# Kernel tuning notes

Measured on AMD Instinct MI355X. Metric: run time of the kernel, lower is better.

Reference implementation:

```python
import jax, jax.numpy as jnp
import numpy as np

HID, AA, ESM = 128, 21, 320
D1 = HID + AA + ESM          # 469
N_GRAPHS = 64
BN_EPS = 1e-5


def _lin_params(key, din, dout):
    k1, k2 = jax.random.split(key)
    s = 1.0 / np.sqrt(din)
    W = jax.random.uniform(k1, (din, dout), jnp.float32, -s, s)
    b = jax.random.uniform(k2, (dout,), jnp.float32, -s, s)
    return W, b


def setup_inputs() -> dict:
    key = jax.random.key(0)
    ks = jax.random.split(key, 16)
    N, E = 30000, 480000
    inp = {
        'prot_x': jax.random.normal(ks[0], (N, 6485), jnp.float32),
        'prot_edge_index': jax.random.randint(ks[1], (2, E), 0, N, jnp.int64),
        'prot_batch': jnp.sort(jax.random.randint(ks[2], (N,), 0, N_GRAPHS, jnp.int64)),
    }
    inp['fl1_W'], inp['fl1_b'] = _lin_params(ks[3], 6165 - 21, HID)
    inp['fl2_W'], inp['fl2_b'] = _lin_params(ks[4], AA, AA)
    inp['fl3_W'], inp['fl3_b'] = _lin_params(ks[5], ESM, ESM)
    inp['pdb1_W'], inp['pdb1_b'] = _lin_params(ks[6], D1, D1)
    inp['pdb2_W'], inp['pdb2_b'] = _lin_params(ks[7], D1, 2 * D1)
    inp['af1_W'], inp['af1_b'] = _lin_params(ks[8], D1, D1)
    inp['af2_W'], inp['af2_b'] = _lin_params(ks[9], D1, 2 * D1)
    inp['pdb3_W'], inp['pdb3_b'] = _lin_params(ks[10], 4 * D1, 4 * D1)
    inp['fc1_W'], inp['fc1_b'] = _lin_params(ks[11], 4 * D1, 1024)
    inp['bn_g'] = jnp.ones((1024,), jnp.float32)
    inp['bn_b'] = jnp.zeros((1024,), jnp.float32)
    inp['fc2_W'], inp['fc2_b'] = _lin_params(ks[12], 1024, 486)
    return inp


def _gcn_graph(edge_index, n):
    # add self-loops, symmetric normalization D^-1/2 (A+I) D^-1/2
    loops = jnp.arange(n, dtype=edge_index.dtype)
    src = jnp.concatenate([edge_index[0], loops])
    dst = jnp.concatenate([edge_index[1], loops])
    deg = jax.ops.segment_sum(jnp.ones_like(dst, jnp.float32), dst, n)
    dinv = jax.lax.rsqrt(jnp.maximum(deg, 1.0))  # deg >= 1 via self-loop
    norm = dinv[src] * dinv[dst]
    return src, dst, norm


def _gcn_conv(x, W, b, src, dst, norm, n):
    h = x @ W                                   # [N, Dout]
    msg = h[src] * norm[:, None]                # gather + scale
    return jax.ops.segment_sum(msg, dst, n) + b  # scatter-add


def reference(prot_x, prot_edge_index, prot_batch,
              fl1_W, fl1_b, fl2_W, fl2_b, fl3_W, fl3_b,
              pdb1_W, pdb1_b, pdb2_W, pdb2_b,
              af1_W, af1_b, af2_W, af2_b,
              pdb3_W, pdb3_b, fc1_W, fc1_b, bn_g, bn_b, fc2_W, fc2_b):
    n = prot_x.shape[0]
    relu = jax.nn.relu
    f1 = relu(prot_x[:, 21:6165] @ fl1_W + fl1_b)   # [N,128]
    f2 = relu(prot_x[:, :21] @ fl2_W + fl2_b)       # [N,21]
    f3 = relu(prot_x[:, 6165:] @ fl3_W + fl3_b)     # [N,320]
    feat = jnp.concatenate([f2, f1, f3], axis=1)    # [N,469]

    src, dst, norm = _gcn_graph(prot_edge_index, n)
    x = relu(_gcn_conv(feat, pdb1_W, pdb1_b, src, dst, norm, n))
    x = relu(_gcn_conv(x, pdb2_W, pdb2_b, src, dst, norm, n))
    y = relu(_gcn_conv(feat, af1_W, af1_b, src, dst, norm, n))
    y = relu(_gcn_conv(y, af2_W, af2_b, src, dst, norm, n))
    z = jnp.concatenate([x, y], axis=1)             # [N, 4*469]
    z = relu(_gcn_conv(z, pdb3_W, pdb3_b, src, dst, norm, n))

    # gap: global mean pool per graph
    cnt = jax.ops.segment_sum(jnp.ones((n,), jnp.float32), prot_batch, N_GRAPHS)
    z = jax.ops.segment_sum(z, prot_batch, N_GRAPHS) / jnp.maximum(cnt, 1.0)[:, None]

    z = z @ fc1_W + fc1_b                            # [G,1024]
    mu = jnp.mean(z, axis=0)
    var = jnp.mean((z - mu) ** 2, axis=0)            # biased, torch BN training math
    z = (z - mu) * jax.lax.rsqrt(var + BN_EPS) * bn_g + bn_b
    z = relu(z)                                      # dropout = identity (eval)
    z = z @ fc2_W + fc2_b
    return jax.nn.sigmoid(z)
```

## Files before the change

kernel.cpp:

```cpp
#include <hip/hip_runtime.h>
#include <hip/hip_bf16.h>
#include <stdint.h>

#define NG 64

typedef __attribute__((ext_vector_type(8))) short bf16x8;
typedef __attribute__((ext_vector_type(4))) float f32x4;

#define AS1 __attribute__((address_space(1)))
#define AS3 __attribute__((address_space(3)))

static __device__ __forceinline__ unsigned short f2b(float f) {
    unsigned u = __float_as_uint(f);
    return (unsigned short)((u + 0x7fffu + ((u >> 16) & 1u)) >> 16);
}
static __device__ __forceinline__ float b2f(unsigned short h) {
    return __uint_as_float(((unsigned)h) << 16);
}
static __device__ __forceinline__ void gl16(const void* g, void* l) {
    __builtin_amdgcn_global_load_lds(
        (const AS1 void*)(uintptr_t)g,
        (AS3 void*)(unsigned)(uintptr_t)l, 16, 0, 0);
}

__global__ void initdeg_k(float* deg, int* cnt, int n) {
    int i = blockIdx.x * blockDim.x + threadIdx.x;
    if (i < n) { deg[i] = 1.0f; cnt[i] = 0; }
}
__global__ void count_k(const int* __restrict__ dst, float* deg, int* cnt, int E) {
    int e = blockIdx.x * blockDim.x + threadIdx.x;
    if (e < E) { int d = dst[e]; atomicAdd(&deg[d], 1.0f); atomicAdd(&cnt[d], 1); }
}
__global__ void dinv_k(const float* __restrict__ deg, float* dinv, int n) {
    int i = blockIdx.x * blockDim.x + threadIdx.x;
    if (i < n) dinv[i] = rsqrtf(fmaxf(deg[i], 1.0f));
}
__global__ void exscan_k(const int* __restrict__ cnt, int* rowptr, int n) {
    __shared__ int tmp[1024];
    __shared__ int carry;
    int tid = threadIdx.x;
    if (tid == 0) { carry = 0; rowptr[0] = 0; }
    __syncthreads();
    for (int base = 0; base < n; base += 1024) {
        int i = base + tid;
        int v = (i < n) ? cnt[i] : 0;
        tmp[tid] = v;
        __syncthreads();
        for (int off = 1; off < 1024; off <<= 1) {
            int t = (tid >= off) ? tmp[tid - off] : 0;
            __syncthreads();
            tmp[tid] += t;
            __syncthreads();
        }
        int inc = tmp[tid] + carry;
        if (i < n) rowptr[i + 1] = inc;
        __syncthreads();
        if (tid == 1023) carry = inc;
        __syncthreads();
    }
}
__global__ void fillinit_k(const int* __restrict__ rowptr, int* fill, int n) {
    int i = blockIdx.x * blockDim.x + threadIdx.x;
    if (i < n) fill[i] = rowptr[i];
}
__global__ void fill_k(const int* __restrict__ src, const int* __restrict__ dst,
                       int* fill, int* csr, int E) {
    int e = blockIdx.x * blockDim.x + threadIdx.x;
    if (e < E) {
        int d = dst[e];
        int pos = atomicAdd(&fill[d], 1);
        csr[pos] = src[e];
    }
}

__global__ void cvt_k(const float* __restrict__ x, int ldx, int c0,
                      unsigned short* __restrict__ out, int K) {
    int kc = blockIdx.x * blockDim.x + threadIdx.x;
    int row = blockIdx.y;
    if (kc * 8 >= K) return;
    const float* src = x + (size_t)row * ldx + c0 + kc * 8;
    unsigned short t[8];
#pragma unroll
    for (int i = 0; i < 8; ++i) t[i] = f2b(src[i]);
    *(bf16x8*)(out + (size_t)row * K + kc * 8) = *(const bf16x8*)t;
}

__global__ void wtconv_k(const float* __restrict__ W, int K, int Nout,
                         unsigned short* __restrict__ Wt, int Kpad) {
    __shared__ float t[32][33];
    int k0 = blockIdx.x * 32, n0 = blockIdx.y * 32;
    int cx = threadIdx.x & 31, ry = threadIdx.x >> 5;
#pragma unroll
    for (int p = 0; p < 4; ++p) {
        int k = k0 + ry + p * 8, nn = n0 + cx;
        t[ry + p * 8][cx] = (k < K && nn < Nout) ? W[(size_t)k * Nout + nn] : 0.0f;
    }
    __syncthreads();
#pragma unroll
    for (int p = 0; p < 4; ++p) {
        int nn = n0 + ry + p * 8, k = k0 + cx;
        Wt[(size_t)nn * Kpad + k] = f2b(t[cx][ry + p * 8]);
    }
}

__global__ void fl2_k(const float* __restrict__ x, int ldx,
                      const float* __restrict__ W, const float* __restrict__ b,
                      unsigned short* __restrict__ out, int ldo, int n) {
    __shared__ float Ws[441];
    __shared__ float Bs[21];
    int tid = threadIdx.x;
    for (int i = tid; i < 441; i += 256) Ws[i] = W[i];
    if (tid < 21) Bs[tid] = b[tid];
    __syncthreads();
    int row = blockIdx.x * 256 + tid;
    if (row >= n) return;
    float xv[21];
#pragma unroll
    for (int j = 0; j < 21; ++j) xv[j] = x[(size_t)row * ldx + j];
    for (int c = 0; c < 21; ++c) {
        float a = Bs[c];
#pragma unroll
        for (int j = 0; j < 21; ++j) a = fmaf(xv[j], Ws[j * 21 + c], a);
        out[(size_t)row * ldo + c] = f2b(fmaxf(a, 0.0f));
    }
}

__global__ __launch_bounds__(256) void mgemm_k(
    const unsigned short* __restrict__ A, int lda,
    const unsigned short* __restrict__ Bt, int ldb,
    const float* __restrict__ bias,
    unsigned short* __restrict__ C, int ldc, int coff,
    int K, int Nout, int Nzero) {
    __shared__ unsigned short As[128 * 32];
    __shared__ unsigned short Bs[128 * 32];
    const int tid = threadIdx.x;
    const int w = tid >> 6, lane = tid & 63;
    const int m0 = blockIdx.y * 128, n0 = blockIdx.x * 128;
    const int wr = w >> 1, wc = w & 1;

    f32x4 acc[4][4];
#pragma unroll
    for (int i = 0; i < 4; ++i)
#pragma unroll
        for (int j = 0; j < 4; ++j) acc[i][j] = (f32x4){0.f, 0.f, 0.f, 0.f};

    const int ko = (lane >> 4) * 8;
    const int rA = wr * 64 + (lane & 15);
    const int rB = wc * 64 + (lane & 15);

    for (int k0 = 0; k0 < K; k0 += 32) {
#pragma unroll
        for (int j = 0; j < 2; ++j) {
            int c = w * 2 + j;
            int idx = c * 64 + lane;
            int row = idx >> 2, cc = idx & 3;
            gl16(A + (size_t)(m0 + row) * lda + k0 + cc * 8, &As[c * 512]);
            gl16(Bt + (size_t)(n0 + row) * ldb + k0 + cc * 8, &Bs[c * 512]);
        }
        __syncthreads();
        bf16x8 a[4], b[4];
#pragma unroll
        for (int i = 0; i < 4; ++i) {
            a[i] = *(const bf16x8*)&As[(rA + i * 16) * 32 + ko];
            b[i] = *(const bf16x8*)&Bs[(rB + i * 16) * 32 + ko];
        }
#pragma unroll
        for (int i = 0; i < 4; ++i)
#pragma unroll
            for (int j = 0; j < 4; ++j)
                acc[i][j] = __builtin_amdgcn_mfma_f32_16x16x32_bf16(a[i], b[j], acc[i][j], 0, 0, 0);
        __syncthreads();
    }

    const int cn = lane & 15, r4 = (lane >> 4) * 4;
    for (int ni = 0; ni < 4; ++ni) {
        int col = n0 + wc * 64 + ni * 16 + cn;
        if (col >= Nzero) continue;
        bool real = col < Nout;
        float bb = real ? bias[col] : 0.0f;
#pragma unroll
        for (int mi = 0; mi < 4; ++mi) {
#pragma unroll
            for (int r = 0; r < 4; ++r) {
                int row = m0 + wr * 64 + mi * 16 + r4 + r;
                float x = real ? fmaxf(acc[mi][ni][r] + bb, 0.0f) : 0.0f;
                C[(size_t)row * ldc + coff + col] = f2b(x);
            }
        }
    }
}

__global__ __launch_bounds__(256) void agg_wave_k(
    const unsigned short* __restrict__ in, unsigned short* __restrict__ out,
    const float* __restrict__ dinv, const int* __restrict__ rowptr,
    const int* __restrict__ csr, int D8, int ld, int n) {
    int lane = threadIdx.x & 63;
    int node = blockIdx.x * 4 + (threadIdx.x >> 6);
    if (node >= n) return;
    bool act = lane < D8;
    float di = dinv[node];
    float acc[8];
#pragma unroll
    for (int t = 0; t < 8; ++t) acc[t] = 0.0f;
    if (act) {
        bf16x8 v = *(const bf16x8*)(in + (size_t)node * ld + lane * 8);
#pragma unroll
        for (int t = 0; t < 8; ++t) acc[t] = di * b2f((unsigned short)v[t]);
    }
    int s = rowptr[node], e = rowptr[node + 1];
    for (int j = s; j < e; ++j) {
        int src = csr[j];
        float wgt = dinv[src];
        if (act) {
            bf16x8 v = *(const bf16x8*)(in + (size_t)src * ld + lane * 8);
#pragma unroll
            for (int t = 0; t < 8; ++t) acc[t] = fmaf(wgt, b2f((unsigned short)v[t]), acc[t]);
        }
    }
    if (act) {
        unsigned short o[8];
#pragma unroll
        for (int t = 0; t < 8; ++t) o[t] = f2b(di * acc[t]);
        *(bf16x8*)(out + (size_t)node * ld + lane * 8) = *(const bf16x8*)o;
    }
}

__global__ __launch_bounds__(256) void agg_block_k(
    const unsigned short* __restrict__ in, unsigned short* __restrict__ out,
    const float* __restrict__ dinv, const int* __restrict__ rowptr,
    const int* __restrict__ csr, int D8, int ld, int n) {
    int i = blockIdx.x;
    int tid = threadIdx.x;
    __shared__ int s_src[64];
    __shared__ float s_w[64];
    bool act = tid < D8;
    float di = dinv[i];
    float acc[8];
#pragma unroll
    for (int t = 0; t < 8; ++t) acc[t] = 0.0f;
    if (act) {
        bf16x8 v = *(const bf16x8*)(in + (size_t)i * ld + tid * 8);
#pragma unroll
        for (int t = 0; t < 8; ++t) acc[t] = di * b2f((unsigned short)v[t]);
    }
    int s = rowptr[i], e = rowptr[i + 1];
    for (int c = s; c < e; c += 64) {
        int k = c + tid;
        if (tid < 64 && k < e) { int sn = csr[k]; s_src[tid] = sn; s_w[tid] = dinv[sn]; }
        __syncthreads();
        int m = e - c; if (m > 64) m = 64;
        for (int j = 0; j < m; ++j) {
            int sn = s_src[j];
            float wgt = s_w[j];
            if (act) {
                bf16x8 v = *(const bf16x8*)(in + (size_t)sn * ld + tid * 8);
#pragma unroll
                for (int t = 0; t < 8; ++t) acc[t] = fmaf(wgt, b2f((unsigned short)v[t]), acc[t]);
            }
        }
        __syncthreads();
    }
    if (act) {
        unsigned short o[8];
#pragma unroll
        for (int t = 0; t < 8; ++t) o[t] = f2b(di * acc[t]);
        *(bf16x8*)(out + (size_t)i * ld + tid * 8) = *(const bf16x8*)o;
    }
}

__global__ void pool_k(const unsigned short* __restrict__ in, int ld,
                       const int* __restrict__ batch,
                       float* __restrict__ out, int n, int D) {
    int g = blockIdx.y;
    int d = blockIdx.x * blockDim.x + threadIdx.x;
    if (d >= D) return;
    int lo = 0, hi = n;
    while (lo < hi) { int mid = (lo + hi) >> 1; if (batch[mid] < g) lo = mid + 1; else hi = mid; }
    int start = lo;
    lo = start; hi = n;
    while (lo < hi) { int mid = (lo + hi) >> 1; if (batch[mid] < g + 1) lo = mid + 1; else hi = mid; }
    int end = lo;
    float sum = 0.0f;
    for (int r = start; r < end; r++) sum += b2f(in[(size_t)r * ld + d]);
    out[(size_t)g * D + d] = sum / fmaxf((float)(end - start), 1.0f);
}

__global__ __launch_bounds__(256) void sgemm_part_k(
    const float* __restrict__ A, int lda,
    const float* __restrict__ W, int ldw,
    float* __restrict__ part, int K, int Nout, int ksplit) {
    const int n0 = blockIdx.x * 64;
    const int ks = blockIdx.y;
    const int kbeg = (int)(((long long)K * ks) / ksplit);
    const int kend = (int)(((long long)K * (ks + 1)) / ksplit);
    const int tx = threadIdx.x & 63, ty = threadIdx.x >> 6;
    __shared__ float As[64][65];
    float acc[16];
#pragma unroll
    for (int r = 0; r < 16; ++r) acc[r] = 0.0f;

    for (int kb = kbeg; kb < kend; kb += 64) {
        int kc = kend - kb; if (kc > 64) kc = 64;
        for (int i = threadIdx.x; i < 64 * 64; i += 256) {
            int r = i >> 6, c = i & 63;
            As[r][c] = (c < kc) ? A[(size_t)r * lda + kb + c] : 0.0f;
        }
        __syncthreads();
        if (n0 + tx < Nout) {
            for (int k = 0; k < kc; ++k) {
                float w = W[(size_t)(kb + k) * ldw + n0 + tx];
#pragma unroll
                for (int r = 0; r < 16; ++r)
                    acc[r] = fmaf(As[ty * 16 + r][k], w, acc[r]);
            }
        }
        __syncthreads();
    }
    if (n0 + tx < Nout) {
#pragma unroll
        for (int r = 0; r < 16; ++r)
            part[((size_t)ks * 64 + ty * 16 + r) * Nout + n0 + tx] = acc[r];
    }
}

__global__ void sgemm_reduce_k(const float* __restrict__ part, const float* __restrict__ bias,
                               float* __restrict__ C, int ldc, int Nout, int ksplit, int act) {
    int i = blockIdx.x * blockDim.x + threadIdx.x;
    if (i >= NG * Nout) return;
    int m = i / Nout, n = i - m * Nout;
    float v = bias[n];
    for (int s = 0; s < ksplit; ++s) v += part[((size_t)s * 64 + m) * Nout + n];
    if (act == 2) v = 1.0f / (1.0f + expf(-v));
    C[(size_t)m * ldc + n] = v;
}

__global__ void bn_stats_k(const float* __restrict__ z, float* mu, float* var) {
    int c = blockIdx.x * blockDim.x + threadIdx.x;
    if (c >= 1024) return;
    float s = 0.0f, s2 = 0.0f;
    for (int r = 0; r < NG; r++) { float v = z[r * 1024 + c]; s += v; s2 += v * v; }
    float m = s / (float)NG;
    mu[c] = m;
    var[c] = s2 / (float)NG - m * m;
}
__global__ void bn_apply_k(const float* __restrict__ z, const float* __restrict__ mu,
                           const float* __restrict__ var, const float* __restrict__ g,
                           const float* __restrict__ b, float* __restrict__ outb) {
    int i = blockIdx.x * blockDim.x + threadIdx.x;
    if (i >= NG * 1024) return;
    int c = i & 1023;
    float v = (z[i] - mu[c]) * rsqrtf(var[c] + 1e-5f) * g[c] + b[c];
    outb[i] = fmaxf(v, 0.0f);
}

extern "C" void kernel_launch(void* const* d_in, const int* in_sizes, int n_in,
                              void* d_out, int out_size, void* d_ws, size_t ws_size,
                              hipStream_t stream) {
    (void)n_in; (void)out_size; (void)ws_size;
    const float* prot_x = (const float*)d_in[0];
    const int*   eidx   = (const int*)d_in[1];
    const int*   batch  = (const int*)d_in[2];
    const float* fl1_W = (const float*)d_in[3],  *fl1_b = (const float*)d_in[4];
    const float* fl2_W = (const float*)d_in[5],  *fl2_b = (const float*)d_in[6];
    const float* fl3_W = (const float*)d_in[7],  *fl3_b = (const float*)d_in[8];
    const float* pdb1_W = (const float*)d_in[9],  *pdb1_b = (const float*)d_in[10];
    const float* pdb2_W = (const float*)d_in[11], *pdb2_b = (const float*)d_in[12];
    const float* af1_W  = (const float*)d_in[13], *af1_b  = (const float*)d_in[14];
    const float* af2_W  = (const float*)d_in[15], *af2_b  = (const float*)d_in[16];
    const float* pdb3_W = (const float*)d_in[17], *pdb3_b = (const float*)d_in[18];
    const float* fc1_W  = (const float*)d_in[19], *fc1_b  = (const float*)d_in[20];
    const float* bn_g   = (const float*)d_in[21], *bn_b   = (const float*)d_in[22];
    const float* fc2_W  = (const float*)d_in[23], *fc2_b  = (const float*)d_in[24];

    const int N = in_sizes[2];
    const int E = in_sizes[1] / 2;
    const int* e_src = eidx;
    const int* e_dst = eidx + E;
    const int Mpad = ((N + 127) / 128) * 128;

    char* wp = (char*)d_ws;
    auto alloc = [&](size_t bytes) -> char* {
        char* r = wp; wp += (bytes + 255) & ~(size_t)255; return r;
    };
    unsigned short* feat = (unsigned short*)alloc((size_t)Mpad * 480 * 2);
    unsigned short* tmpb = (unsigned short*)alloc((size_t)Mpad * 480 * 2);
    unsigned short* hx   = (unsigned short*)alloc((size_t)Mpad * 480 * 2);
    unsigned short* hy   = (unsigned short*)alloc((size_t)Mpad * 480 * 2);
    size_t r0a = (size_t)Mpad * 6144 * 2, r0b = (size_t)Mpad * 1888 * 2 * 2;
    char* region0 = alloc(r0a > r0b ? r0a : r0b);
    unsigned short* xb1  = (unsigned short*)region0;
    unsigned short* zb   = (unsigned short*)region0;
    unsigned short* zagg = (unsigned short*)(region0 + (size_t)Mpad * 1888 * 2);
    unsigned short* xb3  = (unsigned short*)alloc((size_t)Mpad * 320 * 2);
    unsigned short* wt_fl1  = (unsigned short*)alloc((size_t)128 * 6144 * 2);
    unsigned short* wt_fl3  = (unsigned short*)alloc((size_t)384 * 320 * 2);
    unsigned short* wt_pdb1 = (unsigned short*)alloc((size_t)512 * 480 * 2);
    unsigned short* wt_af1  = (unsigned short*)alloc((size_t)512 * 480 * 2);
    unsigned short* wt_pdb2 = (unsigned short*)alloc((size_t)1024 * 480 * 2);
    unsigned short* wt_af2  = (unsigned short*)alloc((size_t)1024 * 480 * 2);
    unsigned short* wt_pdb3 = (unsigned short*)alloc((size_t)1920 * 1888 * 2);
    float* f_deg  = (float*)alloc((size_t)N * 4);
    float* f_dinv = (float*)alloc((size_t)N * 4);
    float* f_pool = (float*)alloc((size_t)NG * 1876 * 4);
    float* f_fc1  = (float*)alloc((size_t)NG * 1024 * 4);
    float* f_bn   = (float*)alloc((size_t)NG * 1024 * 4);
    float* f_mu   = (float*)alloc(1024 * 4);
    float* f_var  = (float*)alloc(1024 * 4);
    float* f_part = (float*)alloc((size_t)16 * 64 * 1024 * 4);
    int* i_cnt    = (int*)alloc((size_t)N * 4);
    int* i_rowptr = (int*)alloc((size_t)(N + 1) * 4);
    int* i_fill   = (int*)alloc((size_t)N * 4);
    int* i_csr    = (int*)alloc((size_t)E * 4);

    auto mg = [&](const unsigned short* A, int lda, const unsigned short* Wt, int ldb,
                  const float* bias, unsigned short* C, int ldc, int coff,
                  int K, int Nout, int Nzero) {
        dim3 g((Nout + 127) / 128, Mpad / 128);
        mgemm_k<<<g, 256, 0, stream>>>(A, lda, Wt, ldb, bias, C, ldc, coff, K, Nout, Nzero);
    };
    auto wt = [&](const float* W, int K, int Nout, unsigned short* Wt, int Kpad) {
        int Ntile = ((Nout + 127) / 128) * 128;
        wtconv_k<<<dim3(Kpad / 32, Ntile / 32), 256, 0, stream>>>(W, K, Nout, Wt, Kpad);
    };

    initdeg_k<<<(N + 255) / 256, 256, 0, stream>>>(f_deg, i_cnt, N);
    count_k<<<(E + 255) / 256, 256, 0, stream>>>(e_dst, f_deg, i_cnt, E);
    dinv_k<<<(N + 255) / 256, 256, 0, stream>>>(f_deg, f_dinv, N);
    exscan_k<<<1, 1024, 0, stream>>>(i_cnt, i_rowptr, N);
    fillinit_k<<<(N + 255) / 256, 256, 0, stream>>>(i_rowptr, i_fill, N);
    fill_k<<<(E + 255) / 256, 256, 0, stream>>>(e_src, e_dst, i_fill, i_csr, E);

    wt(fl1_W, 6144, 128, wt_fl1, 6144);
    wt(fl3_W, 320, 320, wt_fl3, 320);
    wt(pdb1_W, 469, 469, wt_pdb1, 480);
    wt(af1_W, 469, 469, wt_af1, 480);
    wt(pdb2_W, 469, 938, wt_pdb2, 480);
    wt(af2_W, 469, 938, wt_af2, 480);
    wt(pdb3_W, 1876, 1876, wt_pdb3, 1888);

    cvt_k<<<dim3(3, N), 256, 0, stream>>>(prot_x, 6485, 21, xb1, 6144);
    cvt_k<<<dim3(1, N), 256, 0, stream>>>(prot_x, 6485, 6165, xb3, 320);

    fl2_k<<<(N + 255) / 256, 256, 0, stream>>>(prot_x, 6485, fl2_W, fl2_b, feat, 480, N);
    mg(xb1, 6144, wt_fl1, 6144, fl1_b, feat, 480, 21, 6144, 128, 128);
    mg(xb3, 320, wt_fl3, 320, fl3_b, feat, 480, 149, 320, 320, 331);

    agg_wave_k<<<(N + 3) / 4, 256, 0, stream>>>(feat, tmpb, f_dinv, i_rowptr, i_csr, 60, 480, N);
    mg(tmpb, 480, wt_pdb1, 480, pdb1_b, hx, 480, 0, 480, 469, 480);
    mg(tmpb, 480, wt_af1, 480, af1_b, hy, 480, 0, 480, 469, 480);
    agg_wave_k<<<(N + 3) / 4, 256, 0, stream>>>(hx, tmpb, f_dinv, i_rowptr, i_csr, 60, 480, N);
    mg(tmpb, 480, wt_pdb2, 480, pdb2_b, zb, 1888, 0, 480, 938, 938);
    agg_wave_k<<<(N + 3) / 4, 256, 0, stream>>>(hy, tmpb, f_dinv, i_rowptr, i_csr, 60, 480, N);
    mg(tmpb, 480, wt_af2, 480, af2_b, zb, 1888, 938, 480, 938, 950);
    agg_block_k<<<N, 256, 0, stream>>>(zb, zagg, f_dinv, i_rowptr, i_csr, 236, 1888, N);
    mg(zagg, 1888, wt_pdb3, 1888, pdb3_b, zb, 1888, 0, 1888, 1876, 1888);

    pool_k<<<dim3((1876 + 255) / 256, NG), 256, 0, stream>>>(zb, 1888, batch, f_pool, N, 1876);
    sgemm_part_k<<<dim3(16, 16), 256, 0, stream>>>(f_pool, 1876, fc1_W, 1024, f_part, 1876, 1024, 16);
    sgemm_reduce_k<<<(NG * 1024 + 255) / 256, 256, 0, stream>>>(f_part, fc1_b, f_fc1, 1024, 1024, 16, 0);
    bn_stats_k<<<4, 256, 0, stream>>>(f_fc1, f_mu, f_var);
    bn_apply_k<<<(NG * 1024 + 255) / 256, 256, 0, stream>>>(f_fc1, f_mu, f_var, bn_g, bn_b, f_bn);
    sgemm_part_k<<<dim3(8, 16), 256, 0, stream>>>(f_bn, 1024, fc2_W, 486, f_part, 1024, 486, 16);
    sgemm_reduce_k<<<(NG * 486 + 255) / 256, 256, 0, stream>>>(f_part, fc2_b, (float*)d_out, 486, 486, 16, 2);
}
```

Before: 1.913 ms.

## Fuse fp32 input conversion into GEMM, swizzle tiles, and streamline graph prep kernels

Removes the separate fp32-to-bf16 conversion passes over the large input by loading fp32 rows directly into the GEMM and converting them in registers, with a 64-wide N tile for the narrow first-layer GEMMs. Adds XCD-aware block swizzling to the GEMM grid and drops wasted column tiles by sizing the grid from Nzero. It also batches CSR index and weight loads per wave with shuffles in the aggregation, replaces the LDS scan with a wave-shuffle scan, drops the float degree atomics, and fuses the two BatchNorm kernels. The fused A path gives up the async global-to-LDS loads and clamps rows past N, which adds register and ALU work inside the GEMM.

```diff
diff --git a/kernel.cpp b/kernel.cpp
--- a/kernel.cpp
+++ b/kernel.cpp
@@ -23,39 +23,48 @@
         (AS3 void*)(unsigned)(uintptr_t)l, 16, 0, 0);
 }
 
-__global__ void initdeg_k(float* deg, int* cnt, int n) {
+__global__ void initcnt_k(int* cnt, int n) {
     int i = blockIdx.x * blockDim.x + threadIdx.x;
-    if (i < n) { deg[i] = 1.0f; cnt[i] = 0; }
-}
-__global__ void count_k(const int* __restrict__ dst, float* deg, int* cnt, int E) {
+    if (i < n) cnt[i] = 0;
+}
+__global__ void count_k(const int* __restrict__ dst, int* cnt, int E) {
     int e = blockIdx.x * blockDim.x + threadIdx.x;
-    if (e < E) { int d = dst[e]; atomicAdd(&deg[d], 1.0f); atomicAdd(&cnt[d], 1); }
-}
-__global__ void dinv_k(const float* __restrict__ deg, float* dinv, int n) {
+    if (e < E) atomicAdd(&cnt[dst[e]], 1);
+}
+__global__ void dinv_k(const int* __restrict__ cnt, float* dinv, int n) {
     int i = blockIdx.x * blockDim.x + threadIdx.x;
-    if (i < n) dinv[i] = rsqrtf(fmaxf(deg[i], 1.0f));
+    if (i < n) dinv[i] = rsqrtf((float)(cnt[i] + 1));
 }
 __global__ void exscan_k(const int* __restrict__ cnt, int* rowptr, int n) {
-    __shared__ int tmp[1024];
+    __shared__ int wsum[16];
     __shared__ int carry;
-    int tid = threadIdx.x;
+    int tid = threadIdx.x, lane = tid & 63, wid = tid >> 6;
     if (tid == 0) { carry = 0; rowptr[0] = 0; }
     __syncthreads();
     for (int base = 0; base < n; base += 1024) {
         int i = base + tid;
-        int v = (i < n) ? cnt[i] : 0;
-        tmp[tid] = v;
-        __syncthreads();
-        for (int off = 1; off < 1024; off <<= 1) {
-            int t = (tid >= off) ? tmp[tid - off] : 0;
-            __syncthreads();
-            tmp[tid] += t;
-            __syncthreads();
-        }
-        int inc = tmp[tid] + carry;
-        if (i < n) rowptr[i + 1] = inc;
-        __syncthreads();
-        if (tid == 1023) carry = inc;
+        int x = (i < n) ? cnt[i] : 0;
+#pragma unroll
+        for (int off = 1; off < 64; off <<= 1) {
+            int t = __shfl_up(x, off);
+            if (lane >= off) x += t;
+        }
+        if (lane == 63) wsum[wid] = x;
+        __syncthreads();
+        if (tid < 16) {
+            int s = wsum[tid];
+#pragma unroll
+            for (int off = 1; off < 16; off <<= 1) {
+                int t = __shfl_up(s, off);
+                if (tid >= off) s += t;
+            }
+            wsum[tid] = s;
+        }
+        __syncthreads();
+        int add = carry + (wid ? wsum[wid - 1] : 0);
+        if (i < n) rowptr[i + 1] = x + add;
+        __syncthreads();
+        if (tid == 1023) carry = x + add;
         __syncthreads();
     }
 }
@@ -71,18 +80,6 @@
         int pos = atomicAdd(&fill[d], 1);
         csr[pos] = src[e];
     }
-}
-
-__global__ void cvt_k(const float* __restrict__ x, int ldx, int c0,
-                      unsigned short* __restrict__ out, int K) {
-    int kc = blockIdx.x * blockDim.x + threadIdx.x;
-    int row = blockIdx.y;
-    if (kc * 8 >= K) return;
-    const float* src = x + (size_t)row * ldx + c0 + kc * 8;
-    unsigned short t[8];
-#pragma unroll
-    for (int i = 0; i < 8; ++i) t[i] = f2b(src[i]);
-    *(bf16x8*)(out + (size_t)row * K + kc * 8) = *(const bf16x8*)t;
 }
 
 __global__ void wtconv_k(const float* __restrict__ W, int K, int Nout,
@@ -125,65 +122,96 @@
     }
 }
 
-__global__ __launch_bounds__(256) void mgemm_k(
-    const unsigned short* __restrict__ A, int lda,
+template<int BNT, bool A32>
+__global__ __launch_bounds__(256) void mgemm_t(
+    const void* __restrict__ Aptr, int lda, int Mreal,
     const unsigned short* __restrict__ Bt, int ldb,
     const float* __restrict__ bias,
     unsigned short* __restrict__ C, int ldc, int coff,
-    int K, int Nout, int Nzero) {
+    int K, int Nout, int Nzero, int GX) {
+    constexpr int NI = BNT / 32;
     __shared__ unsigned short As[128 * 32];
-    __shared__ unsigned short Bs[128 * 32];
+    __shared__ unsigned short Bs[BNT * 32];
     const int tid = threadIdx.x;
     const int w = tid >> 6, lane = tid & 63;
-    const int m0 = blockIdx.y * 128, n0 = blockIdx.x * 128;
+
+    const int nwg = gridDim.x;
+    const int q = nwg >> 3, r = nwg & 7;
+    const int xcd = blockIdx.x & 7, oidx = blockIdx.x >> 3;
+    const int swz = (xcd < r ? xcd * (q + 1) : r * (q + 1) + (xcd - r) * q) + oidx;
+    const int m0 = (swz / GX) * 128, n0 = (swz % GX) * BNT;
+
     const int wr = w >> 1, wc = w & 1;
 
-    f32x4 acc[4][4];
+    f32x4 acc[4][NI];
 #pragma unroll
     for (int i = 0; i < 4; ++i)
 #pragma unroll
-        for (int j = 0; j < 4; ++j) acc[i][j] = (f32x4){0.f, 0.f, 0.f, 0.f};
+        for (int j = 0; j < NI; ++j) acc[i][j] = (f32x4){0.f, 0.f, 0.f, 0.f};
 
     const int ko = (lane >> 4) * 8;
     const int rA = wr * 64 + (lane & 15);
-    const int rB = wc * 64 + (lane & 15);
+    const int rB = wc * (BNT / 2) + (lane & 15);
 
     for (int k0 = 0; k0 < K; k0 += 32) {
-#pragma unroll
-        for (int j = 0; j < 2; ++j) {
-            int c = w * 2 + j;
-            int idx = c * 64 + lane;
-            int row = idx >> 2, cc = idx & 3;
-            gl16(A + (size_t)(m0 + row) * lda + k0 + cc * 8, &As[c * 512]);
+        if constexpr (A32) {
+            const float* Af = (const float*)Aptr;
+#pragma unroll
+            for (int j = 0; j < 2; ++j) {
+                int c = w * 2 + j;
+                int id2 = c * 64 + lane;
+                int row = id2 >> 2, cc = id2 & 3;
+                int gm = m0 + row; if (gm > Mreal - 1) gm = Mreal - 1;
+                const float* ap = Af + (size_t)gm * lda + k0 + cc * 8;
+                float4 v0 = *(const float4*)ap;
+                float4 v1 = *(const float4*)(ap + 4);
+                unsigned short t[8] = {f2b(v0.x), f2b(v0.y), f2b(v0.z), f2b(v0.w),
+                                       f2b(v1.x), f2b(v1.y), f2b(v1.z), f2b(v1.w)};
+                *(bf16x8*)&As[row * 32 + cc * 8] = *(const bf16x8*)t;
+            }
+        } else {
+            const unsigned short* Ab = (const unsigned short*)Aptr;
+#pragma unroll
+            for (int j = 0; j < 2; ++j) {
+                int c = w * 2 + j;
+                int id2 = c * 64 + lane;
+                int row = id2 >> 2, cc = id2 & 3;
+                gl16(Ab + (size_t)(m0 + row) * lda + k0 + cc * 8, &As[c * 512]);
+            }
+        }
+#pragma unroll
+        for (int j = 0; j < BNT / 64; ++j) {
+            int c = w * (BNT / 64) + j;
+            int id2 = c * 64 + lane;
+            int row = id2 >> 2, cc = id2 & 3;
             gl16(Bt + (size_t)(n0 + row) * ldb + k0 + cc * 8, &Bs[c * 512]);
         }
         __syncthreads();
-        bf16x8 a[4], b[4];
-#pragma unroll
-        for (int i = 0; i < 4; ++i) {
-            a[i] = *(const bf16x8*)&As[(rA + i * 16) * 32 + ko];
-            b[i] = *(const bf16x8*)&Bs[(rB + i * 16) * 32 + ko];
-        }
+        bf16x8 a[4], b[NI];
+#pragma unroll
+        for (int i = 0; i < 4; ++i) a[i] = *(const bf16x8*)&As[(rA + i * 16) * 32 + ko];
+#pragma unroll
+        for (int j = 0; j < NI; ++j) b[j] = *(const bf16x8*)&Bs[(rB + j * 16) * 32 + ko];
 #pragma unroll
         for (int i = 0; i < 4; ++i)
 #pragma unroll
-            for (int j = 0; j < 4; ++j)
+            for (int j = 0; j < NI; ++j)
                 acc[i][j] = __builtin_amdgcn_mfma_f32_16x16x32_bf16(a[i], b[j], acc[i][j], 0, 0, 0);
         __syncthreads();
     }
 
     const int cn = lane & 15, r4 = (lane >> 4) * 4;
-    for (int ni = 0; ni < 4; ++ni) {
-        int col = n0 + wc * 64 + ni * 16 + cn;
+    for (int ni = 0; ni < NI; ++ni) {
+        int col = n0 + wc * (BNT / 2) + ni * 16 + cn;
         if (col >= Nzero) continue;
         bool real = col < Nout;
         float bb = real ? bias[col] : 0.0f;
 #pragma unroll
         for (int mi = 0; mi < 4; ++mi) {
 #pragma unroll
-            for (int r = 0; r < 4; ++r) {
-                int row = m0 + wr * 64 + mi * 16 + r4 + r;
-                float x = real ? fmaxf(acc[mi][ni][r] + bb, 0.0f) : 0.0f;
+            for (int rr = 0; rr < 4; ++rr) {
+                int row = m0 + wr * 64 + mi * 16 + r4 + rr;
+                float x = real ? fmaxf(acc[mi][ni][rr] + bb, 0.0f) : 0.0f;
                 C[(size_t)row * ldc + coff + col] = f2b(x);
             }
         }
@@ -208,13 +236,18 @@
         for (int t = 0; t < 8; ++t) acc[t] = di * b2f((unsigned short)v[t]);
     }
     int s = rowptr[node], e = rowptr[node + 1];
-    for (int j = s; j < e; ++j) {
-        int src = csr[j];
-        float wgt = dinv[src];
-        if (act) {
-            bf16x8 v = *(const bf16x8*)(in + (size_t)src * ld + lane * 8);
-#pragma unroll
-            for (int t = 0; t < 8; ++t) acc[t] = fmaf(wgt, b2f((unsigned short)v[t]), acc[t]);
+    for (int c = s; c < e; c += 64) {
+        int m = e - c; if (m > 64) m = 64;
+        int idx = (c + lane < e) ? csr[c + lane] : 0;
+        float wl = dinv[idx];
+        for (int j = 0; j < m; ++j) {
+            int src = __shfl(idx, j);
+            float wgt = __shfl(wl, j);
+            if (act) {
+                bf16x8 v = *(const bf16x8*)(in + (size_t)src * ld + lane * 8);
+#pragma unroll
+                for (int t = 0; t < 8; ++t) acc[t] = fmaf(wgt, b2f((unsigned short)v[t]), acc[t]);
+            }
         }
     }
     if (act) {
@@ -334,23 +367,18 @@
     C[(size_t)m * ldc + n] = v;
 }
 
-__global__ void bn_stats_k(const float* __restrict__ z, float* mu, float* var) {
+__global__ void bn_k(const float* __restrict__ z, const float* __restrict__ g,
+                     const float* __restrict__ b, float* __restrict__ out) {
     int c = blockIdx.x * blockDim.x + threadIdx.x;
     if (c >= 1024) return;
     float s = 0.0f, s2 = 0.0f;
     for (int r = 0; r < NG; r++) { float v = z[r * 1024 + c]; s += v; s2 += v * v; }
-    float m = s / (float)NG;
-    mu[c] = m;
-    var[c] = s2 / (float)NG - m * m;
-}
-__global__ void bn_apply_k(const float* __restrict__ z, const float* __restrict__ mu,
-                           const float* __restrict__ var, const float* __restrict__ g,
-                           const float* __restrict__ b, float* __restrict__ outb) {
-    int i = blockIdx.x * blockDim.x + threadIdx.x;
-    if (i >= NG * 1024) return;
-    int c = i & 1023;
-    float v = (z[i] - mu[c]) * rsqrtf(var[c] + 1e-5f) * g[c] + b[c];
-    outb[i] = fmaxf(v, 0.0f);
+    float mu = s / (float)NG;
+    float var = s2 / (float)NG - mu * mu;
+    float sc = g[c] * rsqrtf(var + 1e-5f);
+    float sh = b[c] - mu * sc;
+    for (int r = 0; r < NG; r++)
+        out[r * 1024 + c] = fmaxf(fmaf(z[r * 1024 + c], sc, sh), 0.0f);
 }
 
 extern "C" void kernel_launch(void* const* d_in, const int* in_sizes, int n_in,
@@ -386,12 +414,8 @@
     unsigned short* tmpb = (unsigned short*)alloc((size_t)Mpad * 480 * 2);
     unsigned short* hx   = (unsigned short*)alloc((size_t)Mpad * 480 * 2);
     unsigned short* hy   = (unsigned short*)alloc((size_t)Mpad * 480 * 2);
-    size_t r0a = (size_t)Mpad * 6144 * 2, r0b = (size_t)Mpad * 1888 * 2 * 2;
-    char* region0 = alloc(r0a > r0b ? r0a : r0b);
-    unsigned short* xb1  = (unsigned short*)region0;
-    unsigned short* zb   = (unsigned short*)region0;
-    unsigned short* zagg = (unsigned short*)(region0 + (size_t)Mpad * 1888 * 2);
-    unsigned short* xb3  = (unsigned short*)alloc((size_t)Mpad * 320 * 2);
+    unsigned short* zb   = (unsigned short*)alloc((size_t)Mpad * 1888 * 2);
+    unsigned short* zagg = (unsigned short*)alloc((size_t)Mpad * 1888 * 2);
     unsigned short* wt_fl1  = (unsigned short*)alloc((size_t)128 * 6144 * 2);
     unsigned short* wt_fl3  = (unsigned short*)alloc((size_t)384 * 320 * 2);
     unsigned short* wt_pdb1 = (unsigned short*)alloc((size_t)512 * 480 * 2);
@@ -399,33 +423,38 @@
     unsigned short* wt_pdb2 = (unsigned short*)alloc((size_t)1024 * 480 * 2);
     unsigned short* wt_af2  = (unsigned short*)alloc((size_t)1024 * 480 * 2);
     unsigned short* wt_pdb3 = (unsigned short*)alloc((size_t)1920 * 1888 * 2);
-    float* f_deg  = (float*)alloc((size_t)N * 4);
     float* f_dinv = (float*)alloc((size_t)N * 4);
     float* f_pool = (float*)alloc((size_t)NG * 1876 * 4);
     float* f_fc1  = (float*)alloc((size_t)NG * 1024 * 4);
     float* f_bn   = (float*)alloc((size_t)NG * 1024 * 4);
-    float* f_mu   = (float*)alloc(1024 * 4);
-    float* f_var  = (float*)alloc(1024 * 4);
     float* f_part = (float*)alloc((size_t)16 * 64 * 1024 * 4);
     int* i_cnt    = (int*)alloc((size_t)N * 4);
     int* i_rowptr = (int*)alloc((size_t)(N + 1) * 4);
     int* i_fill   = (int*)alloc((size_t)N * 4);
     int* i_csr    = (int*)alloc((size_t)E * 4);
 
-    auto mg = [&](const unsigned short* A, int lda, const unsigned short* Wt, int ldb,
-                  const float* bias, unsigned short* C, int ldc, int coff,
-                  int K, int Nout, int Nzero) {
-        dim3 g((Nout + 127) / 128, Mpad / 128);
-        mgemm_k<<<g, 256, 0, stream>>>(A, lda, Wt, ldb, bias, C, ldc, coff, K, Nout, Nzero);
+    auto mg128 = [&](const unsigned short* A, int lda, const unsigned short* Wt, int ldb,
+                     const float* bias, unsigned short* C, int ldc, int coff,
+                     int K, int Nout, int Nzero) {
+        int gx = (Nzero + 127) / 128;
+        mgemm_t<128, false><<<gx * (Mpad / 128), 256, 0, stream>>>(
+            A, lda, Mpad, Wt, ldb, bias, C, ldc, coff, K, Nout, Nzero, gx);
+    };
+    auto mg64f = [&](const float* A, int lda, const unsigned short* Wt, int ldb,
+                     const float* bias, unsigned short* C, int ldc, int coff,
+                     int K, int Nout, int Nzero) {
+        int gx = (Nzero + 63) / 64;
+        mgemm_t<64, true><<<gx * (Mpad / 128), 256, 0, stream>>>(
+            A, lda, N, Wt, ldb, bias, C, ldc, coff, K, Nout, Nzero, gx);
     };
     auto wt = [&](const float* W, int K, int Nout, unsigned short* Wt, int Kpad) {
         int Ntile = ((Nout + 127) / 128) * 128;
         wtconv_k<<<dim3(Kpad / 32, Ntile / 32), 256, 0, stream>>>(W, K, Nout, Wt, Kpad);
     };
 
-    initdeg_k<<<(N + 255) / 256, 256, 0, stream>>>(f_deg, i_cnt, N);
-    count_k<<<(E + 255) / 256, 256, 0, stream>>>(e_dst, f_deg, i_cnt, E);
-    dinv_k<<<(N + 255) / 256, 256, 0, stream>>>(f_deg, f_dinv, N);
+    initcnt_k<<<(N + 255) / 256, 256, 0, stream>>>(i_cnt, N);
+    count_k<<<(E + 255) / 256, 256, 0, stream>>>(e_dst, i_cnt, E);
+    dinv_k<<<(N + 255) / 256, 256, 0, stream>>>(i_cnt, f_dinv, N);
     exscan_k<<<1, 1024, 0, stream>>>(i_cnt, i_rowptr, N);
     fillinit_k<<<(N + 255) / 256, 256, 0, stream>>>(i_rowptr, i_fill, N);
     fill_k<<<(E + 255) / 256, 256, 0, stream>>>(e_src, e_dst, i_fill, i_csr, E);
@@ -438,28 +467,24 @@
     wt(af2_W, 469, 938, wt_af2, 480);
     wt(pdb3_W, 1876, 1876, wt_pdb3, 1888);
 
-    cvt_k<<<dim3(3, N), 256, 0, stream>>>(prot_x, 6485, 21, xb1, 6144);
-    cvt_k<<<dim3(1, N), 256, 0, stream>>>(prot_x, 6485, 6165, xb3, 320);
-
     fl2_k<<<(N + 255) / 256, 256, 0, stream>>>(prot_x, 6485, fl2_W, fl2_b, feat, 480, N);
-    mg(xb1, 6144, wt_fl1, 6144, fl1_b, feat, 480, 21, 6144, 128, 128);
-    mg(xb3, 320, wt_fl3, 320, fl3_b, feat, 480, 149, 320, 320, 331);
+    mg64f(prot_x + 21,   6485, wt_fl1, 6144, fl1_b, feat, 480, 21,  6144, 128, 128);
+    mg64f(prot_x + 6165, 6485, wt_fl3, 320,  fl3_b, feat, 480, 149, 320,  320, 331);
 
     agg_wave_k<<<(N + 3) / 4, 256, 0, stream>>>(feat, tmpb, f_dinv, i_rowptr, i_csr, 60, 480, N);
-    mg(tmpb, 480, wt_pdb1, 480, pdb1_b, hx, 480, 0, 480, 469, 480);
-    mg(tmpb, 480, wt_af1, 480, af1_b, hy, 480, 0, 480, 469, 480);
+    mg128(tmpb, 480, wt_pdb1, 480, pdb1_b, hx, 480, 0, 480, 469, 480);
+    mg128(tmpb, 480, wt_af1, 480, af1_b, hy, 480, 0, 480, 469, 480);
     agg_wave_k<<<(N + 3) / 4, 256, 0, stream>>>(hx, tmpb, f_dinv, i_rowptr, i_csr, 60, 480, N);
-    mg(tmpb, 480, wt_pdb2, 480, pdb2_b, zb, 1888, 0, 480, 938, 938);
+    mg128(tmpb, 480, wt_pdb2, 480, pdb2_b, zb, 1888, 0, 480, 938, 938);
     agg_wave_k<<<(N + 3) / 4, 256, 0, stream>>>(hy, tmpb, f_dinv, i_rowptr, i_csr, 60, 480, N);
-    mg(tmpb, 480, wt_af2, 480, af2_b, zb, 1888, 938, 480, 938, 950);
+    mg128(tmpb, 480, wt_af2, 480, af2_b, zb, 1888, 938, 480, 938, 950);
     agg_block_k<<<N, 256, 0, stream>>>(zb, zagg, f_dinv, i_rowptr, i_csr, 236, 1888, N);
-    mg(zagg, 1888, wt_pdb3, 1888, pdb3_b, zb, 1888, 0, 1888, 1876, 1888);
+    mg128(zagg, 1888, wt_pdb3, 1888, pdb3_b, zb, 1888, 0, 1888, 1876, 1888);
 
     pool_k<<<dim3((1876 + 255) / 256, NG), 256, 0, stream>>>(zb, 1888, batch, f_pool, N, 1876);
     sgemm_part_k<<<dim3(16, 16), 256, 0, stream>>>(f_pool, 1876, fc1_W, 1024, f_part, 1876, 1024, 16);
     sgemm_reduce_k<<<(NG * 1024 + 255) / 256, 256, 0, stream>>>(f_part, fc1_b, f_fc1, 1024, 1024, 16, 0);
-    bn_stats_k<<<4, 256, 0, stream>>>(f_fc1, f_mu, f_var);
-    bn_apply_k<<<(NG * 1024 + 255) / 256, 256, 0, stream>>>(f_fc1, f_mu, f_var, bn_g, bn_b, f_bn);
+    bn_k<<<4, 256, 0, stream>>>(f_fc1, bn_g, bn_b, f_bn);
     sgemm_part_k<<<dim3(8, 16), 256, 0, stream>>>(f_bn, 1024, fc2_W, 486, f_part, 1024, 486, 16);
     sgemm_reduce_k<<<(NG * 486 + 255) / 256, 256, 0, stream>>>(f_part, fc2_b, (float*)d_out, 486, 486, 16, 2);
 }
```

After: 1.801 ms. 5.9% less time.
